# Optimization experiments

Hardware: AMD Instinct MI355X
Metric: run time of the kernel (lower is better)

Reference implementation:

```python
import jax, jax.numpy as jnp
import numpy as np

D_MODEL, D_K, D_V, H = 512, 64, 64, 8
B, NQ, NK = 2, 2048, 2048


def setup_inputs() -> dict:
    key = jax.random.key(0)
    ks = jax.random.split(key, 12)
    inp = {
        "queries": jax.random.normal(ks[0], (B, NQ, D_MODEL), jnp.float32),
        "keys": jax.random.normal(ks[1], (B, NK, D_MODEL), jnp.float32),
        "values": jax.random.normal(ks[2], (B, NK, D_MODEL), jnp.float32),
        "attention_weights": jax.random.uniform(ks[3], (B, H, NQ, NK), jnp.float32),
        # causal mask: True above the diagonal => masked (every row keeps >=1 entry)
        "attention_mask": jnp.broadcast_to(
            jnp.triu(jnp.ones((NQ, NK), dtype=bool), k=1), (B, H, NQ, NK)
        ),
        # linear params, torch Linear convention: W [out, in], b [out]
        "Wq": 0.001 * jax.random.normal(ks[4], (H * D_K, D_MODEL), jnp.float32),
        "bq": jnp.zeros((H * D_K,), jnp.float32),
        "Wk": 0.001 * jax.random.normal(ks[5], (H * D_K, D_MODEL), jnp.float32),
        "bk": jnp.zeros((H * D_K,), jnp.float32),
        "Wv": 0.001 * jax.random.normal(ks[6], (H * D_V, D_MODEL), jnp.float32),
        "bv": jnp.zeros((H * D_V,), jnp.float32),
        "Wo": 0.001 * jax.random.normal(ks[7], (D_MODEL, H * D_V), jnp.float32),
        "bo": jnp.zeros((D_MODEL,), jnp.float32),
    }
    return inp


def reference(queries, keys, values, attention_weights, attention_mask,
              Wq, bq, Wk, bk, Wv, bv, Wo, bo):
    b_s, nq, _ = queries.shape
    nk = keys.shape[1]
    # projections -> (b, h, n, d)
    q = (queries @ Wq.T + bq).reshape(b_s, nq, H, D_K).transpose(0, 2, 1, 3)
    k = (keys @ Wk.T + bk).reshape(b_s, nk, H, D_K).transpose(0, 2, 1, 3)
    v = (values @ Wv.T + bv).reshape(b_s, nk, H, D_V).transpose(0, 2, 1, 3)
    att = jnp.einsum('bhqd,bhkd->bhqk', q, k) / np.sqrt(D_K).astype(np.float32)
    att = att * attention_weights
    att = jnp.where(attention_mask, -jnp.inf, att)
    att = jax.nn.softmax(att, axis=-1)  # dropout p=0 => identity (eval)
    out = jnp.einsum('bhqk,bhkd->bhqd', att, v)
    out = out.transpose(0, 2, 1, 3).reshape(b_s, nq, H * D_V)
    return out @ Wo.T + bo
```

## Files before the change

kernel.cpp:

```cpp
#include <hip/hip_runtime.h>


typedef unsigned short u16;
typedef unsigned int u32;
typedef __bf16 bf16x8 __attribute__((ext_vector_type(8)));
typedef float f32x4 __attribute__((ext_vector_type(4)));

#define NQTILES 32

__device__ inline u16 f2bf(float f) {
    u32 x = __builtin_bit_cast(u32, f);
    u32 r = (x + 0x7fffu + ((x >> 16) & 1u)) >> 16;
    return (u16)r;
}

__device__ inline f32x4 mfma16(bf16x8 a, bf16x8 b, f32x4 c) {
    return __builtin_amdgcn_mfma_f32_16x16x32_bf16(a, b, c, 0, 0, 0);
}

__device__ inline void gload16(const void* g, void* l) {
    __builtin_amdgcn_global_load_lds((const __attribute__((address_space(1))) void*)g,
                                     (__attribute__((address_space(3))) void*)l, 16, 0, 0);
}

__device__ inline void stage_swz(const u16* __restrict__ src, int ld, int nrows,
                                 char* lds, int tid) {
    int lane = tid & 63;
    int total = nrows * 8;
    for (int p = tid; p < total; p += 256) {
        int row = p >> 3;
        int seg = (p & 7) ^ (row & 7);
        const char* g = (const char*)(src + (size_t)row * ld) + (seg << 4);
        char* l = lds + ((size_t)(p - lane) << 4);
        gload16(g, l);
    }
}

__device__ inline bf16x8 ldsf(const char* lds, int row, int seg) {
    return *(const bf16x8*)(lds + row * 128 + (((seg ^ (row & 7)) & 7) << 4));
}

__global__ __launch_bounds__(256) void convert_kernel(
    const float* __restrict__ q, const float* __restrict__ k, const float* __restrict__ v,
    const float* __restrict__ wq, const float* __restrict__ wk, const float* __restrict__ wv,
    const float* __restrict__ wo, u16* __restrict__ dst) {
    size_t i = ((size_t)blockIdx.x * 256 + threadIdx.x) * 8;
    if (i >= 7340032) return;
    const float* src; size_t off;
    if      (i < 2097152) { src = q;  off = i; }
    else if (i < 4194304) { src = k;  off = i - 2097152; }
    else if (i < 6291456) { src = v;  off = i - 4194304; }
    else if (i < 6553600) { src = wq; off = i - 6291456; }
    else if (i < 6815744) { src = wk; off = i - 6553600; }
    else if (i < 7077888) { src = wv; off = i - 6815744; }
    else                  { src = wo; off = i - 7077888; }
    float4 a = *(const float4*)(src + off);
    float4 b = *(const float4*)(src + off + 4);
    uint4 pk;
    pk.x = f2bf(a.x) | ((u32)f2bf(a.y) << 16);
    pk.y = f2bf(a.z) | ((u32)f2bf(a.w) << 16);
    pk.z = f2bf(b.x) | ((u32)f2bf(b.y) << 16);
    pk.w = f2bf(b.z) | ((u32)f2bf(b.w) << 16);
    *(uint4*)(dst + i) = pk;
}

__device__ inline void gemm_core(const u16* __restrict__ A, const u16* __restrict__ W,
                                 const float* __restrict__ bias,
                                 u16* __restrict__ outB, float* __restrict__ outF,
                                 char* Alds, char* Blds, int bx, int by, int tid) {
    const int lane = tid & 63, wid = tid >> 6;
    const int wr = wid >> 1, wc = wid & 1;
    const int lg = lane >> 4, lc = lane & 15;
    const int brow = by * 128, bcol = bx * 128;
    f32x4 acc[4][4] = {};
    for (int kt = 0; kt < 8; ++kt) {
        stage_swz(A + (size_t)brow * 512 + kt * 64, 512, 128, Alds, tid);
        stage_swz(W + (size_t)bcol * 512 + kt * 64, 512, 128, Blds, tid);
        __syncthreads();
#pragma unroll
        for (int s = 0; s < 2; ++s) {
            bf16x8 af[4], bf[4];
#pragma unroll
            for (int m = 0; m < 4; ++m) af[m] = ldsf(Alds, wr * 64 + m * 16 + lc, s * 4 + lg);
#pragma unroll
            for (int n = 0; n < 4; ++n) bf[n] = ldsf(Blds, wc * 64 + n * 16 + lc, s * 4 + lg);
#pragma unroll
            for (int m = 0; m < 4; ++m)
#pragma unroll
                for (int n = 0; n < 4; ++n)
                    acc[m][n] = mfma16(af[m], bf[n], acc[m][n]);
        }
        __syncthreads();
    }
#pragma unroll
    for (int n = 0; n < 4; ++n) {
        int gcol = bcol + wc * 64 + n * 16 + lc;
        float bv = bias[gcol];
#pragma unroll
        for (int m = 0; m < 4; ++m) {
            int grow0 = brow + wr * 64 + m * 16 + lg * 4;
#pragma unroll
            for (int r = 0; r < 4; ++r) {
                float v = acc[m][n][r] + bv;
                if (outF) outF[(size_t)(grow0 + r) * 512 + gcol] = v;
                else      outB[(size_t)(grow0 + r) * 512 + gcol] = f2bf(v);
            }
        }
    }
}

__global__ __launch_bounds__(256) void gemm_qkv_kernel(
    const u16* __restrict__ qx, const u16* __restrict__ kx, const u16* __restrict__ vx,
    const u16* __restrict__ wq, const u16* __restrict__ wk, const u16* __restrict__ wv,
    const float* __restrict__ bq, const float* __restrict__ bk, const float* __restrict__ bv,
    u16* __restrict__ qp, u16* __restrict__ kp, u16* __restrict__ vp) {
    __shared__ __attribute__((aligned(16))) char Alds[16384];
    __shared__ __attribute__((aligned(16))) char Blds[16384];
    int z = blockIdx.z;
    const u16* A = (z == 0) ? qx : (z == 1) ? kx : vx;
    const u16* W = (z == 0) ? wq : (z == 1) ? wk : wv;
    const float* bias = (z == 0) ? bq : (z == 1) ? bk : bv;
    u16* out = (z == 0) ? qp : (z == 1) ? kp : vp;
    gemm_core(A, W, bias, out, nullptr, Alds, Blds, blockIdx.x, blockIdx.y, threadIdx.x);
}

__global__ __launch_bounds__(256) void gemm_out_kernel(
    const u16* __restrict__ ob, const u16* __restrict__ wo,
    const float* __restrict__ bo, float* __restrict__ out) {
    __shared__ __attribute__((aligned(16))) char Alds[16384];
    __shared__ __attribute__((aligned(16))) char Blds[16384];
    gemm_core(ob, wo, bo, nullptr, out, Alds, Blds, blockIdx.x, blockIdx.y, threadIdx.x);
}

__global__ __launch_bounds__(256) void vtrans_kernel(const u16* __restrict__ vp,
                                                     u16* __restrict__ vt) {
    __shared__ __attribute__((aligned(16))) u16 t[64 * 64];
    int tid = threadIdx.x, lane = tid & 63;
    int nt = blockIdx.x;
    int bh = blockIdx.y;
    int b = bh >> 3, h = bh & 7;
    for (int ii = 0; ii < 2; ++ii) {
        int p = ii * 256 + tid;
        int nrow = p >> 3, seg = p & 7;
        const char* g = (const char*)(vp + ((size_t)(b * 2048 + nt * 64 + nrow)) * 512 + h * 64)
                        + (seg << 4);
        char* l = (char*)t + ((size_t)(p - lane) << 4);
        gload16(g, l);
    }
    __syncthreads();
    for (int ii = 0; ii < 2; ++ii) {
        int idx = ii * 256 + tid;
        int nseg = idx >> 6;
        int d = idx & 63;
        u16 tmp[8];
#pragma unroll
        for (int j = 0; j < 8; ++j) tmp[j] = t[(nseg * 8 + j) * 64 + d];
        uint4 pk;
        pk.x = tmp[0] | ((u32)tmp[1] << 16);
        pk.y = tmp[2] | ((u32)tmp[3] << 16);
        pk.z = tmp[4] | ((u32)tmp[5] << 16);
        pk.w = tmp[6] | ((u32)tmp[7] << 16);
        *(uint4*)(vt + ((size_t)(bh * 64 + d)) * 2048 + nt * 64 + nseg * 8) = pk;
    }
}

__global__ __launch_bounds__(256) void attn_kernel(
    const u16* __restrict__ qp, const u16* __restrict__ kp, const u16* __restrict__ vt,
    const float* __restrict__ wgt, u16* __restrict__ ob) {
    __shared__ __attribute__((aligned(16))) char kbuf[8192];
    __shared__ __attribute__((aligned(16))) char vbuf[8192];
    __shared__ __attribute__((aligned(16))) char pbuf[8192];
    const int tid = threadIdx.x, lane = tid & 63, wid = tid >> 6;
    const int lg = lane >> 4, lc = lane & 15;
    const int bid = blockIdx.x;
    const int rank = bid >> 4;
    const int bh = bid & 15;
    const int it = (NQTILES - 1) - rank;
    const int b = bh >> 3, h = bh & 7;
    const int q0 = it * 64;
    const int wrow = wid * 16;

    stage_swz(qp + ((size_t)(b * 2048 + q0)) * 512 + h * 64, 512, 64, pbuf, tid);
    __syncthreads();
    bf16x8 qf[2];
#pragma unroll
    for (int s = 0; s < 2; ++s) qf[s] = ldsf(pbuf, wrow + lc, s * 4 + lg);

    float mrow[4], lrow[4];
#pragma unroll
    for (int r = 0; r < 4; ++r) { mrow[r] = -1e30f; lrow[r] = 0.f; }
    f32x4 oacc[4] = {};

    const size_t wbase = ((size_t)(b * 8 + h)) * 2048 * 2048;

    for (int j = 0; j <= it; ++j) {
        const int k0 = j * 64;
        stage_swz(kp + ((size_t)(b * 2048 + k0)) * 512 + h * 64, 512, 64, kbuf, tid);
        stage_swz(vt + ((size_t)(bh * 64)) * 2048 + k0, 2048, 64, vbuf, tid);
        float wv[4][4];
#pragma unroll
        for (int c = 0; c < 4; ++c)
#pragma unroll
            for (int r = 0; r < 4; ++r) {
                int qq = q0 + wrow + lg * 4 + r;
                int kk = k0 + c * 16 + lc;
                wv[c][r] = wgt[wbase + (size_t)qq * 2048 + kk];
            }
        __syncthreads();

        f32x4 sacc[4] = {};
#pragma unroll
        for (int s = 0; s < 2; ++s) {
            bf16x8 kf[4];
#pragma unroll
            for (int c = 0; c < 4; ++c) kf[c] = ldsf(kbuf, c * 16 + lc, s * 4 + lg);
#pragma unroll
            for (int c = 0; c < 4; ++c) sacc[c] = mfma16(qf[s], kf[c], sacc[c]);
        }

        float p[4][4];
#pragma unroll
        for (int r = 0; r < 4; ++r) {
            float mx = -1e30f;
#pragma unroll
            for (int c = 0; c < 4; ++c) {
                float sv = sacc[c][r] * 0.125f * wv[c][r];
                if (j == it) {
                    int qq = wrow + lg * 4 + r, kk = c * 16 + lc;
                    if (kk > qq) sv = -1e30f;
                }
                p[c][r] = sv;
                mx = fmaxf(mx, sv);
            }
            mx = fmaxf(mx, __shfl_xor(mx, 1));
            mx = fmaxf(mx, __shfl_xor(mx, 2));
            mx = fmaxf(mx, __shfl_xor(mx, 4));
            mx = fmaxf(mx, __shfl_xor(mx, 8));
            float mnew = fmaxf(mrow[r], mx);
            float sc = __expf(mrow[r] - mnew);
            float sum = 0.f;
#pragma unroll
            for (int c = 0; c < 4; ++c) {
                float e = __expf(p[c][r] - mnew);
                p[c][r] = e;
                sum += e;
            }
            sum += __shfl_xor(sum, 1);
            sum += __shfl_xor(sum, 2);
            sum += __shfl_xor(sum, 4);
            sum += __shfl_xor(sum, 8);
            lrow[r] = lrow[r] * sc + sum;
            mrow[r] = mnew;
#pragma unroll
            for (int c = 0; c < 4; ++c) oacc[c][r] *= sc;
        }

#pragma unroll
        for (int c = 0; c < 4; ++c)
#pragma unroll
            for (int r = 0; r < 4; ++r) {
                int row = wrow + lg * 4 + r;
                int byte = (c * 16 + lc) * 2;
                *(u16*)(pbuf + row * 128 + (byte ^ ((row & 7) << 4))) = f2bf(p[c][r]);
            }

        bf16x8 pa[2];
#pragma unroll
        for (int s = 0; s < 2; ++s) pa[s] = ldsf(pbuf, wrow + lc, s * 4 + lg);
#pragma unroll
        for (int c = 0; c < 4; ++c)
#pragma unroll
            for (int s = 0; s < 2; ++s) {
                bf16x8 vf = ldsf(vbuf, c * 16 + lc, s * 4 + lg);
                oacc[c] = mfma16(pa[s], vf, oacc[c]);
            }
        __syncthreads();
    }

#pragma unroll
    for (int r = 0; r < 4; ++r) {
        float inv = 1.f / lrow[r];
        int qq = q0 + wrow + lg * 4 + r;
        size_t base = ((size_t)(b * 2048 + qq)) * 512 + h * 64;
#pragma unroll
        for (int c = 0; c < 4; ++c)
            ob[base + c * 16 + lc] = f2bf(oacc[c][r] * inv);
    }
}

extern "C" void kernel_launch(void* const* d_in, const int* in_sizes, int n_in,
                              void* d_out, int out_size, void* d_ws, size_t ws_size,
                              hipStream_t stream) {
    const float* q   = (const float*)d_in[0];
    const float* k   = (const float*)d_in[1];
    const float* v   = (const float*)d_in[2];
    const float* wgt = (const float*)d_in[3];
    const float* Wq = (const float*)d_in[5];
    const float* bq = (const float*)d_in[6];
    const float* Wk = (const float*)d_in[7];
    const float* bk = (const float*)d_in[8];
    const float* Wv = (const float*)d_in[9];
    const float* bv = (const float*)d_in[10];
    const float* Wo = (const float*)d_in[11];
    const float* bo = (const float*)d_in[12];
    float* out = (float*)d_out;

    u16* ws  = (u16*)d_ws;
    u16* qx  = ws;
    u16* kx  = qx  + 2097152;
    u16* vx  = kx  + 2097152;
    u16* wqb = vx  + 2097152;
    u16* wkb = wqb + 262144;
    u16* wvb = wkb + 262144;
    u16* wob = wvb + 262144;
    u16* qp  = wob + 262144;
    u16* kp  = qp  + 2097152;
    u16* vp  = kp  + 2097152;
    u16* vtb = vp  + 2097152;
    u16* ob  = vtb + 2097152;

    convert_kernel<<<3584, 256, 0, stream>>>(q, k, v, Wq, Wk, Wv, Wo, qx);
    gemm_qkv_kernel<<<dim3(4, 32, 3), 256, 0, stream>>>(qx, kx, vx, wqb, wkb, wvb,
                                                        bq, bk, bv, qp, kp, vp);
    vtrans_kernel<<<dim3(32, 16), 256, 0, stream>>>(vp, vtb);
    attn_kernel<<<512, 256, 0, stream>>>(qp, kp, vtb, wgt, ob);
    gemm_out_kernel<<<dim3(4, 32, 1), 256, 0, stream>>>(ob, wob, bo, out);
}
```

Measured before the change: 553.4 us.

## Double-buffer LDS tiles in GEMMs and attention, prefetch weights into registers

The QKV and output GEMMs now ping-pong between two LDS buffers, so the next K-tile's global-to-LDS load is issued before the current tile's MFMAs. The attention loop does the same for K and V tiles and prefetches the next block's attention-weight values into registers, hiding global latency behind compute. The V-transpose kernel swaps its thread-to-index mapping so neighbouring threads write contiguous global memory. Launch bounds of 2 blocks per CU are added, which caps registers. LDS use doubles, which could limit occupancy.

After: 541.0 us. -2.2%, faster.

```diff
diff --git a/kernel.cpp b/kernel.cpp
--- a/kernel.cpp
+++ b/kernel.cpp
@@ -38,6 +38,16 @@
 
 __device__ inline bf16x8 ldsf(const char* lds, int row, int seg) {
     return *(const bf16x8*)(lds + row * 128 + (((seg ^ (row & 7)) & 7) << 4));
+}
+
+__device__ inline void loadw(float (&w)[16], const float* __restrict__ wgt, size_t wbase,
+                             int q0, int k0, int wrow, int lg, int lc) {
+#pragma unroll
+    for (int c = 0; c < 4; ++c)
+#pragma unroll
+        for (int r = 0; r < 4; ++r)
+            w[c * 4 + r] =
+                wgt[wbase + (size_t)(q0 + wrow + lg * 4 + r) * 2048 + k0 + c * 16 + lc];
 }
 
 __global__ __launch_bounds__(256) void convert_kernel(
@@ -67,23 +77,29 @@
 __device__ inline void gemm_core(const u16* __restrict__ A, const u16* __restrict__ W,
                                  const float* __restrict__ bias,
                                  u16* __restrict__ outB, float* __restrict__ outF,
-                                 char* Alds, char* Blds, int bx, int by, int tid) {
+                                 char (*Alds)[16384], char (*Blds)[16384],
+                                 int bx, int by, int tid) {
     const int lane = tid & 63, wid = tid >> 6;
     const int wr = wid >> 1, wc = wid & 1;
     const int lg = lane >> 4, lc = lane & 15;
     const int brow = by * 128, bcol = bx * 128;
     f32x4 acc[4][4] = {};
+    stage_swz(A + (size_t)brow * 512, 512, 128, Alds[0], tid);
+    stage_swz(W + (size_t)bcol * 512, 512, 128, Blds[0], tid);
+    __syncthreads();
     for (int kt = 0; kt < 8; ++kt) {
-        stage_swz(A + (size_t)brow * 512 + kt * 64, 512, 128, Alds, tid);
-        stage_swz(W + (size_t)bcol * 512 + kt * 64, 512, 128, Blds, tid);
-        __syncthreads();
+        const int cur = kt & 1;
+        if (kt < 7) {
+            stage_swz(A + (size_t)brow * 512 + (kt + 1) * 64, 512, 128, Alds[cur ^ 1], tid);
+            stage_swz(W + (size_t)bcol * 512 + (kt + 1) * 64, 512, 128, Blds[cur ^ 1], tid);
+        }
 #pragma unroll
         for (int s = 0; s < 2; ++s) {
             bf16x8 af[4], bf[4];
 #pragma unroll
-            for (int m = 0; m < 4; ++m) af[m] = ldsf(Alds, wr * 64 + m * 16 + lc, s * 4 + lg);
-#pragma unroll
-            for (int n = 0; n < 4; ++n) bf[n] = ldsf(Blds, wc * 64 + n * 16 + lc, s * 4 + lg);
+            for (int m = 0; m < 4; ++m) af[m] = ldsf(Alds[cur], wr * 64 + m * 16 + lc, s * 4 + lg);
+#pragma unroll
+            for (int n = 0; n < 4; ++n) bf[n] = ldsf(Blds[cur], wc * 64 + n * 16 + lc, s * 4 + lg);
 #pragma unroll
             for (int m = 0; m < 4; ++m)
 #pragma unroll
@@ -109,13 +125,13 @@
     }
 }
 
-__global__ __launch_bounds__(256) void gemm_qkv_kernel(
+__global__ __launch_bounds__(256, 2) void gemm_qkv_kernel(
     const u16* __restrict__ qx, const u16* __restrict__ kx, const u16* __restrict__ vx,
     const u16* __restrict__ wq, const u16* __restrict__ wk, const u16* __restrict__ wv,
     const float* __restrict__ bq, const float* __restrict__ bk, const float* __restrict__ bv,
     u16* __restrict__ qp, u16* __restrict__ kp, u16* __restrict__ vp) {
-    __shared__ __attribute__((aligned(16))) char Alds[16384];
-    __shared__ __attribute__((aligned(16))) char Blds[16384];
+    __shared__ __attribute__((aligned(16))) char Alds[2][16384];
+    __shared__ __attribute__((aligned(16))) char Blds[2][16384];
     int z = blockIdx.z;
     const u16* A = (z == 0) ? qx : (z == 1) ? kx : vx;
     const u16* W = (z == 0) ? wq : (z == 1) ? wk : wv;
@@ -124,11 +140,11 @@
     gemm_core(A, W, bias, out, nullptr, Alds, Blds, blockIdx.x, blockIdx.y, threadIdx.x);
 }
 
-__global__ __launch_bounds__(256) void gemm_out_kernel(
+__global__ __launch_bounds__(256, 2) void gemm_out_kernel(
     const u16* __restrict__ ob, const u16* __restrict__ wo,
     const float* __restrict__ bo, float* __restrict__ out) {
-    __shared__ __attribute__((aligned(16))) char Alds[16384];
-    __shared__ __attribute__((aligned(16))) char Blds[16384];
+    __shared__ __attribute__((aligned(16))) char Alds[2][16384];
+    __shared__ __attribute__((aligned(16))) char Blds[2][16384];
     gemm_core(ob, wo, bo, nullptr, out, Alds, Blds, blockIdx.x, blockIdx.y, threadIdx.x);
 }
 
@@ -150,8 +166,8 @@
     __syncthreads();
     for (int ii = 0; ii < 2; ++ii) {
         int idx = ii * 256 + tid;
-        int nseg = idx >> 6;
-        int d = idx & 63;
+        int d = idx >> 3;
+        int nseg = idx & 7;
         u16 tmp[8];
 #pragma unroll
         for (int j = 0; j < 8; ++j) tmp[j] = t[(nseg * 8 + j) * 64 + d];
@@ -164,11 +180,11 @@
     }
 }
 
-__global__ __launch_bounds__(256) void attn_kernel(
+__global__ __launch_bounds__(256, 2) void attn_kernel(
     const u16* __restrict__ qp, const u16* __restrict__ kp, const u16* __restrict__ vt,
     const float* __restrict__ wgt, u16* __restrict__ ob) {
-    __shared__ __attribute__((aligned(16))) char kbuf[8192];
-    __shared__ __attribute__((aligned(16))) char vbuf[8192];
+    __shared__ __attribute__((aligned(16))) char kbuf[2][8192];
+    __shared__ __attribute__((aligned(16))) char vbuf[2][8192];
     __shared__ __attribute__((aligned(16))) char pbuf[8192];
     const int tid = threadIdx.x, lane = tid & 63, wid = tid >> 6;
     const int lg = lane >> 4, lc = lane & 15;
@@ -179,8 +195,16 @@
     const int b = bh >> 3, h = bh & 7;
     const int q0 = it * 64;
     const int wrow = wid * 16;
+    const size_t wbase = ((size_t)(b * 8 + h)) * 2048 * 2048;
+    const size_t vtb0 = ((size_t)(bh * 64)) * 2048;
 
     stage_swz(qp + ((size_t)(b * 2048 + q0)) * 512 + h * 64, 512, 64, pbuf, tid);
+    stage_swz(kp + ((size_t)(b * 2048)) * 512 + h * 64, 512, 64, kbuf[0], tid);
+    stage_swz(vt + vtb0, 2048, 64, vbuf[0], tid);
+    float wcur[16], wnxt[16];
+    loadw(wcur, wgt, wbase, q0, 0, wrow, lg, lc);
+#pragma unroll
+    for (int i = 0; i < 16; ++i) wnxt[i] = 0.f;
     __syncthreads();
     bf16x8 qf[2];
 #pragma unroll
@@ -191,45 +215,36 @@
     for (int r = 0; r < 4; ++r) { mrow[r] = -1e30f; lrow[r] = 0.f; }
     f32x4 oacc[4] = {};
 
-    const size_t wbase = ((size_t)(b * 8 + h)) * 2048 * 2048;
-
     for (int j = 0; j <= it; ++j) {
-        const int k0 = j * 64;
-        stage_swz(kp + ((size_t)(b * 2048 + k0)) * 512 + h * 64, 512, 64, kbuf, tid);
-        stage_swz(vt + ((size_t)(bh * 64)) * 2048 + k0, 2048, 64, vbuf, tid);
-        float wv[4][4];
-#pragma unroll
-        for (int c = 0; c < 4; ++c)
-#pragma unroll
-            for (int r = 0; r < 4; ++r) {
-                int qq = q0 + wrow + lg * 4 + r;
-                int kk = k0 + c * 16 + lc;
-                wv[c][r] = wgt[wbase + (size_t)qq * 2048 + kk];
-            }
-        __syncthreads();
+        const int cur = j & 1;
+        if (j < it) {
+            stage_swz(kp + ((size_t)(b * 2048 + (j + 1) * 64)) * 512 + h * 64, 512, 64,
+                      kbuf[cur ^ 1], tid);
+            stage_swz(vt + vtb0 + (j + 1) * 64, 2048, 64, vbuf[cur ^ 1], tid);
+            loadw(wnxt, wgt, wbase, q0, (j + 1) * 64, wrow, lg, lc);
+        }
 
         f32x4 sacc[4] = {};
 #pragma unroll
         for (int s = 0; s < 2; ++s) {
             bf16x8 kf[4];
 #pragma unroll
-            for (int c = 0; c < 4; ++c) kf[c] = ldsf(kbuf, c * 16 + lc, s * 4 + lg);
+            for (int c = 0; c < 4; ++c) kf[c] = ldsf(kbuf[cur], c * 16 + lc, s * 4 + lg);
 #pragma unroll
             for (int c = 0; c < 4; ++c) sacc[c] = mfma16(qf[s], kf[c], sacc[c]);
         }
 
-        float p[4][4];
 #pragma unroll
         for (int r = 0; r < 4; ++r) {
             float mx = -1e30f;
 #pragma unroll
             for (int c = 0; c < 4; ++c) {
-                float sv = sacc[c][r] * 0.125f * wv[c][r];
+                float sv = sacc[c][r] * 0.125f * wcur[c * 4 + r];
                 if (j == it) {
                     int qq = wrow + lg * 4 + r, kk = c * 16 + lc;
                     if (kk > qq) sv = -1e30f;
                 }
-                p[c][r] = sv;
+                sacc[c][r] = sv;
                 mx = fmaxf(mx, sv);
             }
             mx = fmaxf(mx, __shfl_xor(mx, 1));
@@ -241,8 +256,8 @@
             float sum = 0.f;
 #pragma unroll
             for (int c = 0; c < 4; ++c) {
-                float e = __expf(p[c][r] - mnew);
-                p[c][r] = e;
+                float e = __expf(sacc[c][r] - mnew);
+                sacc[c][r] = e;
                 sum += e;
             }
             sum += __shfl_xor(sum, 1);
@@ -261,7 +276,7 @@
             for (int r = 0; r < 4; ++r) {
                 int row = wrow + lg * 4 + r;
                 int byte = (c * 16 + lc) * 2;
-                *(u16*)(pbuf + row * 128 + (byte ^ ((row & 7) << 4))) = f2bf(p[c][r]);
+                *(u16*)(pbuf + row * 128 + (byte ^ ((row & 7) << 4))) = f2bf(sacc[c][r]);
             }
 
         bf16x8 pa[2];
@@ -271,10 +286,14 @@
         for (int c = 0; c < 4; ++c)
 #pragma unroll
             for (int s = 0; s < 2; ++s) {
-                bf16x8 vf = ldsf(vbuf, c * 16 + lc, s * 4 + lg);
+                bf16x8 vf = ldsf(vbuf[cur], c * 16 + lc, s * 4 + lg);
                 oacc[c] = mfma16(pa[s], vf, oacc[c]);
             }
         __syncthreads();
+        if (j < it) {
+#pragma unroll
+            for (int i = 0; i < 16; ++i) wcur[i] = wnxt[i];
+        }
     }
 
 #pragma unroll
```
